# Performance work log

Hardware: AMD Instinct MI355X
Metric: run time of the kernel (lower is better)

## Reference

```python
import jax, jax.numpy as jnp
import numpy as np

B, N, D, V, Y = 4, 2048, 300, 50000, 20000
MAX_REL = 10
LN_EPS = 1e-5


def setup_inputs() -> dict:
    key = jax.random.key(0)
    k1, k2, k3, k4, k5 = jax.random.split(key, 5)
    M_s = jax.random.randint(k1, (B, N), 0, V, dtype=jnp.int64)
    s = 1.0 / np.sqrt(D)
    E_v = jax.random.normal(k2, (V, D), dtype=jnp.float32) * s
    E_v = E_v.at[0].set(0.0)  # padding_idx=0
    E_y = jax.random.normal(k3, (Y, D), dtype=jnp.float32) * s
    E_y = E_y.at[0].set(0.0)
    W_A = jax.random.normal(k4, (D, D), dtype=jnp.float32) * s
    W_O = jax.random.normal(k5, (D, D), dtype=jnp.float32) * s
    gamma = jnp.ones((D,), dtype=jnp.float32)
    beta = jnp.zeros((D,), dtype=jnp.float32)
    return {"M_s": M_s, "E_v": E_v, "E_y": E_y, "W_A": W_A, "W_O": W_O,
            "gamma": gamma, "beta": beta}


def reference(M_s, E_v, E_y, W_A, W_O, gamma, beta):
    # Embedding lookup (dropout is identity in eval / p=0)
    X = E_v[M_s]                                   # [B, N, D]
    Q = X                                          # self-attention mode (v_q=None)
    # weights = Q @ W_A @ X^T
    QW = jnp.einsum('bnd,de->bne', Q, W_A)         # [B, N, D]
    weights = jnp.einsum('bne,bme->bnm', QW, X)    # [B, N, N]
    # relative-distance bias (clipped |i-j|)
    r = jnp.arange(N)
    dist = jnp.clip(jnp.abs(r[None, :] - r[:, None]), 0, MAX_REL).astype(weights.dtype)
    weights = weights - dist
    # padding mask over context (key) positions
    mask = (M_s != 0)                              # [B, N]
    weights = jnp.where(mask[:, None, :], weights, -jnp.inf)
    A = jax.nn.softmax(weights, axis=-1)           # [B, N, N]
    # contextualized query + output projection
    Q_c = jnp.einsum('bnm,bmd->bnd', A, X) @ W_O   # [B, N, D]
    # residual + layernorm over D
    H = Q_c + Q
    mu = jnp.mean(H, axis=-1, keepdims=True)
    var = jnp.mean((H - mu) ** 2, axis=-1, keepdims=True)
    Hn = (H - mu) * jax.lax.rsqrt(var + LN_EPS) * gamma + beta
    # vocab projection over senses
    y_logits = Hn @ E_y.T                          # [B, N, Y]
    return y_logits, A
```

## Files before the change

kernel.cpp:

```cpp
#include <hip/hip_runtime.h>
#include <hip/hip_bf16.h>

#define B_ 4
#define N_ 2048
#define D_ 300
#define Y_ 20000
#define ROWS (B_*N_)

typedef __attribute__((ext_vector_type(8))) short bf16x8;
typedef __attribute__((ext_vector_type(4))) float f32x4;

__device__ __forceinline__ unsigned short f2bf(float f) {
  unsigned u = __float_as_uint(f);
  unsigned r = (u + 0x7FFFu + ((u >> 16) & 1u)) >> 16;
  return (unsigned short)r;
}

__device__ __forceinline__ void gl_lds16(const unsigned short* g, unsigned short* l) {
  __builtin_amdgcn_global_load_lds(
      (const __attribute__((address_space(1))) void*)g,
      (__attribute__((address_space(3))) void*)l, 16, 0, 0);
}

__global__ __launch_bounds__(256) void k_gather_pack(const int* __restrict__ M_s,
    const float* __restrict__ E_v, float* __restrict__ X,
    unsigned short* __restrict__ Xp) {
  __shared__ float xs[320];
  int row = blockIdx.x, tid = threadIdx.x;
  int tok = M_s[row];
  const float* src = E_v + (size_t)tok * D_;
  for (int d = tid; d < 320; d += 256) xs[d] = (d < D_) ? src[d] : 0.f;
  __syncthreads();
  float* dst = X + (size_t)row * D_;
  for (int d = tid; d < D_; d += 256) dst[d] = xs[d];
  if (tid < 40) {
    int kt = tid >> 2, j = tid & 3;
    int tile = row >> 7, fb = (row >> 4) & 7, rl = row & 15;
    unsigned short v[8];
    #pragma unroll
    for (int e = 0; e < 8; ++e) v[e] = f2bf(xs[kt*32 + j*8 + e]);
    size_t off_ = ((size_t)(tile*10 + kt))*4096 + fb*512 + rl*8 + j*128;
    ushort4* o = (ushort4*)&Xp[off_];
    o[0] = make_ushort4(v[0],v[1],v[2],v[3]);
    o[1] = make_ushort4(v[4],v[5],v[6],v[7]);
  }
}

__global__ __launch_bounds__(256) void k_pack(const float* __restrict__ src,
    unsigned short* __restrict__ dst, int nrows, int ncols, int KT) {
  int chunk = blockIdx.x;
  int tile = chunk / KT, kt = chunk - tile*KT;
  size_t obase = (size_t)chunk * 4096;
  #pragma unroll
  for (int p = 0; p < 2; ++p) {
    int idx = p*256 + threadIdx.x;
    int fb = idx >> 6, l = idx & 63;
    int row = tile*128 + fb*16 + (l & 15);
    int gk = kt*32 + (l >> 4)*8;
    unsigned short v[8];
    #pragma unroll
    for (int e = 0; e < 8; ++e) {
      int k = gk + e;
      float f = (row < nrows && k < ncols) ? src[(size_t)row*ncols + k] : 0.f;
      v[e] = f2bf(f);
    }
    ushort4* o = (ushort4*)&dst[obase + (size_t)idx*8];
    o[0] = make_ushort4(v[0],v[1],v[2],v[3]);
    o[1] = make_ushort4(v[4],v[5],v[6],v[7]);
  }
}

__global__ __launch_bounds__(256) void k_packT(const float* __restrict__ src,
    unsigned short* __restrict__ dst, int src_rows, int src_cols, int KT,
    size_t src_bstride, size_t dst_bchunks) {
  __shared__ float ls[32*133];
  int chunk = blockIdx.x, b = blockIdx.y, tid = threadIdx.x;
  const float* s = src + (size_t)b * src_bstride;
  unsigned short* d = dst + ((size_t)b * dst_bchunks + chunk) * 4096;
  int tile = chunk / KT, kt = chunk - tile*KT;
  int c0 = tile*128, k0 = kt*32;
  for (int i = tid; i < 4096; i += 256) {
    int r = i >> 7, c = i & 127;
    int sr = k0 + r, sc = c0 + c;
    ls[r*133 + c] = (sr < src_rows && sc < src_cols) ? s[(size_t)sr*src_cols + sc] : 0.f;
  }
  __syncthreads();
  #pragma unroll
  for (int p = 0; p < 2; ++p) {
    int idx = p*256 + tid;
    int fb = idx >> 6, l = idx & 63;
    int r = fb*16 + (l & 15);
    int kl = (l >> 4)*8;
    unsigned short v[8];
    #pragma unroll
    for (int e = 0; e < 8; ++e) v[e] = f2bf(ls[(kl + e)*133 + r]);
    ushort4* o = (ushort4*)&d[(size_t)idx*8];
    o[0] = make_ushort4(v[0],v[1],v[2],v[3]);
    o[1] = make_ushort4(v[4],v[5],v[6],v[7]);
  }
}

template<int EPI, bool NT, bool SWZ>
__global__ __launch_bounds__(512, 4) void k_gemm256(
    const unsigned short* __restrict__ Ap, const unsigned short* __restrict__ Bp,
    float* __restrict__ out, const int* __restrict__ Ms,
    int MTB, int NTB, int ncols)
{
  __shared__ __align__(16) union {
    unsigned short bstage[10][4096];
    float epi[64*132];
  } sm;
  int nt, mt, z;
  if (SWZ) {
    int wg = blockIdx.x;
    int cpx = (MTB*NTB) >> 3;
    int swz = (wg & 7)*cpx + (wg >> 3);
    mt = swz % MTB; nt = swz / MTB; z = 0;
  } else { nt = blockIdx.x; mt = blockIdx.y; z = blockIdx.z; }
  const int tid = threadIdx.x;
  const int wave = tid >> 6, lane = tid & 63;
  const int wm = wave >> 1, wn = wave & 1;
  const int mtile2 = (z*MTB + mt)*2 + (wm >> 1);
  const unsigned short* Ab = Ap + (size_t)mtile2 * 10 * 4096;
  const unsigned short* Bb = Bp + (size_t)(z*NTB + nt) * 10 * 4096;

  #pragma unroll
  for (int kt = 0; kt < 10; ++kt)
    gl_lds16(Bb + kt*4096 + wave*512 + lane*8, &sm.bstage[kt][wave*512]);

  const unsigned short* ga = Ab + ((wm & 1)*4)*512 + lane*8;
  __syncthreads();

  f32x4 acc[4][4] = {};
  #pragma unroll
  for (int kt = 0; kt < 10; ++kt) {
    bf16x8 a4[4], b4[4];
    #pragma unroll
    for (int i = 0; i < 4; ++i)
      a4[i] = *(const bf16x8*)(ga + kt*4096 + i*512);
    #pragma unroll
    for (int i = 0; i < 4; ++i)
      b4[i] = *(const bf16x8*)&sm.bstage[kt][(wn*4 + i)*512 + lane*8];
    #pragma unroll
    for (int mi = 0; mi < 4; ++mi)
      #pragma unroll
      for (int ni = 0; ni < 4; ++ni)
        acc[mi][ni] = __builtin_amdgcn_mfma_f32_16x16x32_bf16(
            a4[mi], b4[ni], acc[mi][ni], 0, 0, 0);
  }
  __syncthreads();

  const int lr0 = (lane >> 4) << 2;
  const int lc0 = wn*64 + (lane & 15);
  const size_t growbase = ((size_t)(z*MTB + mt)) << 8;
  #pragma unroll
  for (int h = 0; h < 4; ++h) {
    if (wm == h) {
      int tok[4];
      if (EPI == 1) {
        #pragma unroll
        for (int ni = 0; ni < 4; ++ni)
          tok[ni] = Ms[z*N_ + (nt<<7) + lc0 + ni*16];
      }
      #pragma unroll
      for (int mi = 0; mi < 4; ++mi) {
        #pragma unroll
        for (int ni = 0; ni < 4; ++ni) {
          int col = lc0 + ni*16;
          #pragma unroll
          for (int r = 0; r < 4; ++r) {
            int row = lr0 + mi*16 + r;
            float v = acc[mi][ni][r];
            if (EPI == 1) {
              int rb = (mt<<8) + h*64 + row;
              int gc = (nt<<7) + col;
              int dd = rb - gc; if (dd < 0) dd = -dd; if (dd > 10) dd = 10;
              v -= (float)dd;
              if (tok[ni] == 0) v = -3.0e38f;
            }
            sm.epi[row*132 + col] = v;
          }
        }
      }
    }
    __syncthreads();
    {
      const int r0 = tid >> 5;
      const int c4 = (tid & 31) << 2;
      const int gc = (nt << 7) + c4;
      #pragma unroll
      for (int rr = r0; rr < 64; rr += 16) {
        size_t grow = growbase + h*64 + rr;
        if (gc + 3 < ncols) {
          f32x4 v = *(const f32x4*)&sm.epi[rr*132 + c4];
          if (NT) __builtin_nontemporal_store(v, (f32x4*)&out[grow*(size_t)ncols + gc]);
          else    *(f32x4*)&out[grow*(size_t)ncols + gc] = v;
        } else {
          #pragma unroll
          for (int e = 0; e < 4; ++e) {
            int c = gc + e;
            if (c < ncols) {
              float v = sm.epi[rr*132 + c4 + e];
              if (NT) __builtin_nontemporal_store(v, &out[grow*(size_t)ncols + c]);
              else    out[grow*(size_t)ncols + c] = v;
            }
          }
        }
      }
    }
    __syncthreads();
  }
}

template<int EPI, bool NT, bool PACKOUT, bool SWZ>
__global__ __launch_bounds__(256) void k_gemm10(
    const unsigned short* __restrict__ Ap, const unsigned short* __restrict__ Bp,
    float* __restrict__ out, unsigned short* __restrict__ outp,
    const float* __restrict__ resid, const int* __restrict__ Ms,
    int KTd, int MTB, int NTB, int ncols)
{
  __shared__ __align__(16) union {
    unsigned short bstage[10][4096];
    float epi[64*132];
  } sm;
  int nt, mt, z;
  if (SWZ) {
    int nwg = MTB * NTB;
    int wg = blockIdx.x;
    int cpx = nwg >> 3;
    int swz = (wg & 7) * cpx + (wg >> 3);
    mt = swz % MTB; nt = swz / MTB; z = 0;
  } else {
    nt = blockIdx.x; mt = blockIdx.y; z = blockIdx.z;
  }
  const int tid = threadIdx.x;
  const int wave = tid >> 6, lane = tid & 63;
  const int wm = wave >> 1, wn = wave & 1;
  const unsigned short* Ab = Ap + (size_t)(z*MTB + mt) * 10 * 4096;
  const unsigned short* Bb = Bp + (size_t)(z*NTB + nt) * 10 * 4096;

  #pragma unroll
  for (int kt = 0; kt < 10; ++kt) {
    const unsigned short* gb = Bb + kt*4096 + wave*1024 + lane*8;
    unsigned short* lb = &sm.bstage[kt][wave*1024];
    gl_lds16(gb,       lb);
    gl_lds16(gb + 512, lb + 512);
  }

  const unsigned short* ga = Ab + (wm*4)*512 + lane*8;
  bf16x8 aA[4], aB[4];
  #pragma unroll
  for (int i = 0; i < 4; ++i) aA[i] = *(const bf16x8*)(ga + 0*4096 + i*512);
  #pragma unroll
  for (int i = 0; i < 4; ++i) aB[i] = *(const bf16x8*)(ga + 1*4096 + i*512);

  __syncthreads();

  f32x4 acc[4][4] = {};
  auto mfma_step = [&](int kt, const bf16x8* a) {
    bf16x8 bfr[4];
    #pragma unroll
    for (int i = 0; i < 4; ++i)
      bfr[i] = *(const bf16x8*)&sm.bstage[kt][(wn*4 + i)*512 + lane*8];
    #pragma unroll
    for (int mi = 0; mi < 4; ++mi)
      #pragma unroll
      for (int ni = 0; ni < 4; ++ni)
        acc[mi][ni] = __builtin_amdgcn_mfma_f32_16x16x32_bf16(
            a[mi], bfr[ni], acc[mi][ni], 0, 0, 0);
  };
  auto loadA = [&](int kt, bf16x8* d) {
    #pragma unroll
    for (int i = 0; i < 4; ++i) d[i] = *(const bf16x8*)(ga + kt*4096 + i*512);
  };

  #pragma unroll
  for (int kt = 0; kt < 10; kt += 2) {
    mfma_step(kt, aA);
    if (kt + 2 < 10) loadA(kt + 2, aA);
    mfma_step(kt + 1, aB);
    if (kt + 3 < 10) loadA(kt + 3, aB);
  }

  __syncthreads();

  const int lr0 = (lane >> 4) << 2;
  const int lc0 = wn*64 + (lane & 15);
  const size_t growbase = ((size_t)(z*MTB + mt)) << 7;
  #pragma unroll
  for (int h = 0; h < 2; ++h) {
    if (wm == h) {
      int tok[4];
      if (EPI == 1) {
        #pragma unroll
        for (int ni = 0; ni < 4; ++ni)
          tok[ni] = Ms[z*N_ + (nt<<7) + lc0 + ni*16];
      }
      #pragma unroll
      for (int mi = 0; mi < 4; ++mi) {
        #pragma unroll
        for (int ni = 0; ni < 4; ++ni) {
          int col = lc0 + ni*16;
          #pragma unroll
          for (int r = 0; r < 4; ++r) {
            int row = lr0 + mi*16 + r;
            float v = acc[mi][ni][r];
            if (EPI == 1) {
              int rb = (mt<<7) + h*64 + row;
              int gc = (nt<<7) + col;
              int dd = rb - gc; if (dd < 0) dd = -dd; if (dd > 10) dd = 10;
              v -= (float)dd;
              if (tok[ni] == 0) v = -3.0e38f;
            }
            sm.epi[row*132 + col] = v;
          }
        }
      }
    }
    __syncthreads();
    if (PACKOUT) {
      int prow = tid >> 2, pktq = tid & 3;
      int ktd = nt*4 + pktq;
      if (ktd < KTd) {
        int grl = h*64 + prow;
        int fb = grl >> 4, rl = grl & 15;
        size_t cbase = ((size_t)((z*MTB + mt)*KTd + ktd))*4096 + fb*512 + rl*8;
        #pragma unroll
        for (int oct = 0; oct < 4; ++oct) {
          unsigned short v[8];
          #pragma unroll
          for (int e = 0; e < 8; ++e)
            v[e] = f2bf(sm.epi[prow*132 + pktq*32 + oct*8 + e]);
          ushort4* o = (ushort4*)&outp[cbase + oct*128];
          o[0] = make_ushort4(v[0],v[1],v[2],v[3]);
          o[1] = make_ushort4(v[4],v[5],v[6],v[7]);
        }
      }
    } else {
      const int r0 = tid >> 5;
      const int c4 = (tid & 31) << 2;
      const int gc = (nt << 7) + c4;
      #pragma unroll
      for (int rr = r0; rr < 64; rr += 8) {
        size_t grow = growbase + h*64 + rr;
        if (gc + 3 < ncols) {
          f32x4 v = *(const f32x4*)&sm.epi[rr*132 + c4];
          if (EPI == 2) v += *(const f32x4*)&resid[grow*(size_t)ncols + gc];
          if (NT) __builtin_nontemporal_store(v, (f32x4*)&out[grow*(size_t)ncols + gc]);
          else    *(f32x4*)&out[grow*(size_t)ncols + gc] = v;
        } else {
          #pragma unroll
          for (int e = 0; e < 4; ++e) {
            int c = gc + e;
            if (c < ncols) {
              float v = sm.epi[rr*132 + c4 + e];
              if (EPI == 2) v += resid[grow*(size_t)ncols + c];
              if (NT) __builtin_nontemporal_store(v, &out[grow*(size_t)ncols + c]);
              else    out[grow*(size_t)ncols + c] = v;
            }
          }
        }
      }
    }
    __syncthreads();
  }
}

__global__ __launch_bounds__(256) void k_gemm64(
    const unsigned short* __restrict__ Ap, const unsigned short* __restrict__ Bp,
    unsigned short* __restrict__ outp, int KT, int KTd, int MTB, int NTB)
{
  __shared__ __align__(16) union {
    unsigned short stage[2][2][4096];
    float epi[64*132];
  } sm;
  const int nt = blockIdx.x, mt = blockIdx.y, z = blockIdx.z;
  const int tid = threadIdx.x;
  const int wave = tid >> 6, lane = tid & 63;
  const int wm = wave >> 1, wn = wave & 1;
  const unsigned short* Ab = Ap + (size_t)(z*MTB + mt) * KT * 4096;
  const unsigned short* Bb = Bp + (size_t)(z*NTB + nt) * KT * 4096;
  f32x4 acc[4][4] = {};

  auto stage = [&](int s, int kt) {
    const unsigned short* ga = Ab + kt*4096 + wave*1024 + lane*8;
    const unsigned short* gb = Bb + kt*4096 + wave*1024 + lane*8;
    unsigned short* la = &sm.stage[s][0][wave*1024];
    unsigned short* lb = &sm.stage[s][1][wave*1024];
    gl_lds16(ga,       la);
    gl_lds16(ga + 512, la + 512);
    gl_lds16(gb,       lb);
    gl_lds16(gb + 512, lb + 512);
  };

  stage(0, 0);
  __syncthreads();
  for (int kt = 0; kt < KT; ++kt) {
    int cur = kt & 1;
    if (kt + 1 < KT) stage(cur ^ 1, kt + 1);
    bf16x8 af[4], bfr[4];
    #pragma unroll
    for (int i = 0; i < 4; ++i)
      af[i] = *(const bf16x8*)&sm.stage[cur][0][(wm*4 + i)*512 + lane*8];
    #pragma unroll
    for (int i = 0; i < 4; ++i)
      bfr[i] = *(const bf16x8*)&sm.stage[cur][1][(wn*4 + i)*512 + lane*8];
    #pragma unroll
    for (int mi = 0; mi < 4; ++mi)
      #pragma unroll
      for (int ni = 0; ni < 4; ++ni)
        acc[mi][ni] = __builtin_amdgcn_mfma_f32_16x16x32_bf16(
            af[mi], bfr[ni], acc[mi][ni], 0, 0, 0);
    __syncthreads();
  }

  const int lr0 = (lane >> 4) << 2;
  const int lc0 = wn*64 + (lane & 15);
  #pragma unroll
  for (int h = 0; h < 2; ++h) {
    if (wm == h) {
      #pragma unroll
      for (int mi = 0; mi < 4; ++mi)
        #pragma unroll
        for (int ni = 0; ni < 4; ++ni) {
          int col = lc0 + ni*16;
          #pragma unroll
          for (int r = 0; r < 4; ++r)
            sm.epi[(lr0 + mi*16 + r)*132 + col] = acc[mi][ni][r];
        }
    }
    __syncthreads();
    {
      int prow = tid >> 2, pktq = tid & 3;
      int ktd = nt*4 + pktq;
      if (ktd < KTd) {
        int grl = h*64 + prow;
        int fb = grl >> 4, rl = grl & 15;
        size_t cbase = ((size_t)((z*MTB + mt)*KTd + ktd))*4096 + fb*512 + rl*8;
        #pragma unroll
        for (int oct = 0; oct < 4; ++oct) {
          unsigned short v[8];
          #pragma unroll
          for (int e = 0; e < 8; ++e)
            v[e] = f2bf(sm.epi[prow*132 + pktq*32 + oct*8 + e]);
          ushort4* o = (ushort4*)&outp[cbase + oct*128];
          o[0] = make_ushort4(v[0],v[1],v[2],v[3]);
          o[1] = make_ushort4(v[4],v[5],v[6],v[7]);
        }
      }
    }
    __syncthreads();
  }
}

__global__ __launch_bounds__(256) void k_softmax(float* __restrict__ S,
    unsigned short* __restrict__ Apk) {
  __shared__ float w[N_];
  __shared__ float red[4];
  int row = blockIdx.x, tid = threadIdx.x;
  float* sr = S + (size_t)row * N_;
  float vmax = -3.4e38f;
  for (int m = tid; m < N_; m += 256) { float v = sr[m]; w[m] = v; vmax = fmaxf(vmax, v); }
  #pragma unroll
  for (int off = 32; off; off >>= 1) vmax = fmaxf(vmax, __shfl_down(vmax, off, 64));
  if ((tid & 63) == 0) red[tid >> 6] = vmax;
  __syncthreads();
  vmax = fmaxf(fmaxf(red[0], red[1]), fmaxf(red[2], red[3]));
  float vsum = 0.f;
  for (int m = tid; m < N_; m += 256) {
    float e = __expf(w[m] - vmax);
    w[m] = e;
    vsum += e;
  }
  #pragma unroll
  for (int off = 32; off; off >>= 1) vsum += __shfl_down(vsum, off, 64);
  __syncthreads();
  if ((tid & 63) == 0) red[tid >> 6] = vsum;
  __syncthreads();
  float inv = 1.f / ((red[0] + red[1]) + (red[2] + red[3]));
  for (int m = tid; m < N_; m += 256)
    __builtin_nontemporal_store(w[m] * inv, &sr[m]);
  int kt = tid >> 2, j = tid & 3;
  int m0 = kt*32 + j*8;
  int fb = (row >> 4) & 7, rl = row & 15;
  unsigned short v[8];
  #pragma unroll
  for (int e = 0; e < 8; ++e) v[e] = f2bf(w[m0 + e] * inv);
  size_t off_ = ((size_t)((row >> 7)*64 + kt))*4096 + fb*512 + rl*8 + j*128;
  ushort4* o = (ushort4*)&Apk[off_];
  o[0] = make_ushort4(v[0],v[1],v[2],v[3]);
  o[1] = make_ushort4(v[4],v[5],v[6],v[7]);
}

__global__ __launch_bounds__(320) void k_ln_pack(const float* __restrict__ H,
    const float* __restrict__ gamma, const float* __restrict__ beta,
    unsigned short* __restrict__ Hp) {
  __shared__ float red[5];
  __shared__ float hs[320];
  int row = blockIdx.x, tid = threadIdx.x;
  float h = (tid < D_) ? H[(size_t)row*D_ + tid] : 0.f;
  float s = h;
  #pragma unroll
  for (int off = 32; off; off >>= 1) s += __shfl_down(s, off, 64);
  if ((tid & 63) == 0) red[tid >> 6] = s;
  __syncthreads();
  float mu = (red[0]+red[1]+red[2]+red[3]+red[4]) * (1.f/(float)D_);
  float dv = (tid < D_) ? (h - mu) : 0.f;
  float s2 = dv * dv;
  #pragma unroll
  for (int off = 32; off; off >>= 1) s2 += __shfl_down(s2, off, 64);
  __syncthreads();
  if ((tid & 63) == 0) red[tid >> 6] = s2;
  __syncthreads();
  float var = (red[0]+red[1]+red[2]+red[3]+red[4]) * (1.f/(float)D_);
  float rstd = rsqrtf(var + 1e-5f);
  hs[tid] = (tid < D_) ? (dv * rstd * gamma[tid] + beta[tid]) : 0.f;
  __syncthreads();
  if (tid < 40) {
    int kt = tid >> 2, j = tid & 3;
    int tile = row >> 7, fb = (row >> 4) & 7, rl = row & 15;
    unsigned short v[8];
    #pragma unroll
    for (int e = 0; e < 8; ++e) v[e] = f2bf(hs[kt*32 + j*8 + e]);
    size_t off_ = ((size_t)(tile*10 + kt))*4096 + fb*512 + rl*8 + j*128;
    ushort4* o = (ushort4*)&Hp[off_];
    o[0] = make_ushort4(v[0],v[1],v[2],v[3]);
    o[1] = make_ushort4(v[4],v[5],v[6],v[7]);
  }
}

extern "C" void kernel_launch(void* const* d_in, const int* in_sizes, int n_in,
                              void* d_out, int out_size, void* d_ws, size_t ws_size,
                              hipStream_t stream) {
  const int*   M_s   = (const int*)d_in[0];
  const float* E_v   = (const float*)d_in[1];
  const float* E_y   = (const float*)d_in[2];
  const float* W_A   = (const float*)d_in[3];
  const float* W_O   = (const float*)d_in[4];
  const float* gamma = (const float*)d_in[5];
  const float* beta  = (const float*)d_in[6];

  float* Yl = (float*)d_out;
  float* A  = Yl + (size_t)ROWS * Y_;

  float* X  = (float*)d_ws;
  float* QW = X  + (size_t)ROWS * D_;
  float* H  = QW + (size_t)ROWS * D_;
  unsigned short* Ep = (unsigned short*)(H + (size_t)ROWS * D_);
  unsigned short* Hpk = (unsigned short*)X;

  unsigned short* scr = (unsigned short*)(Yl + 100000000ull);
  unsigned short* Xp  = scr;
  unsigned short* QWp = Xp  + 2621440;
  unsigned short* Wap = QWp + 2621440;
  unsigned short* Wop = Wap + 122880;
  unsigned short* XTp = Wop + 122880;
  unsigned short* Cp  = XTp + 3145728;
  unsigned short* Apk = Cp  + 2621440;

  k_gather_pack<<<ROWS, 256, 0, stream>>>(M_s, E_v, X, Xp);
  k_packT <<<dim3(3*10,1), 256, 0, stream>>>(W_A, Wap, D_, D_, 10, 0, 0);
  k_gemm10<0,false,true,false><<<dim3(3,64,1), 256, 0, stream>>>(
      Xp, Wap, nullptr, QWp, nullptr, nullptr, 10, 64, 3, D_);
  k_gemm256<1,false,false><<<dim3(16,8,4), 512, 0, stream>>>(
      QWp, Xp, A, M_s, 8, 16, N_);
  k_softmax<<<ROWS, 256, 0, stream>>>(A, Apk);
  k_packT <<<dim3(3*64,4), 256, 0, stream>>>(X, XTp, N_, D_, 64, (size_t)N_*D_, 192);
  k_gemm64<<<dim3(3,16,4), 256, 0, stream>>>(Apk, XTp, Cp, 64, 10, 16, 3);
  k_packT <<<dim3(3*10,1), 256, 0, stream>>>(W_O, Wop, D_, D_, 10, 0, 0);
  k_gemm10<2,false,false,false><<<dim3(3,64,1), 256, 0, stream>>>(
      Cp, Wop, H, nullptr, X, nullptr, 0, 64, 3, D_);
  k_ln_pack<<<ROWS, 320, 0, stream>>>(H, gamma, beta, Hpk);
  k_pack  <<<157*10, 256, 0, stream>>>(E_y, Ep, Y_, D_, 10);
  k_gemm256<0,true,true><<<dim3(157*32,1,1), 512, 0, stream>>>(
      Hpk, Ep, Yl, nullptr, 32, 157, Y_);
}
```

Measured before the change: 376.0 us.

## Store GEMM epilogue directly from registers and vectorize softmax row handling

The 256-row GEMM epilogue no longer stages the accumulator tile through shared memory with four barrier-separated passes. Each lane now writes its scalar results straight to global memory, which removes the LDS round trip and the barriers but replaces wide coalesced stores with strided scalar stores. The softmax kernel holds each row in registers as two float4 vectors, computes exp once, and uses separate reduction buffers. This drops one barrier and the repeated LDS reads and writes.

```diff
diff --git a/kernel.cpp b/kernel.cpp
--- a/kernel.cpp
+++ b/kernel.cpp
@@ -106,10 +106,7 @@
     float* __restrict__ out, const int* __restrict__ Ms,
     int MTB, int NTB, int ncols)
 {
-  __shared__ __align__(16) union {
-    unsigned short bstage[10][4096];
-    float epi[64*132];
-  } sm;
+  __shared__ __align__(16) unsigned short bstage[10][4096];
   int nt, mt, z;
   if (SWZ) {
     int wg = blockIdx.x;
@@ -126,7 +123,7 @@
 
   #pragma unroll
   for (int kt = 0; kt < 10; ++kt)
-    gl_lds16(Bb + kt*4096 + wave*512 + lane*8, &sm.bstage[kt][wave*512]);
+    gl_lds16(Bb + kt*4096 + wave*512 + lane*8, &bstage[kt][wave*512]);
 
   const unsigned short* ga = Ab + ((wm & 1)*4)*512 + lane*8;
   __syncthreads();
@@ -140,7 +137,7 @@
       a4[i] = *(const bf16x8*)(ga + kt*4096 + i*512);
     #pragma unroll
     for (int i = 0; i < 4; ++i)
-      b4[i] = *(const bf16x8*)&sm.bstage[kt][(wn*4 + i)*512 + lane*8];
+      b4[i] = *(const bf16x8*)&bstage[kt][(wn*4 + i)*512 + lane*8];
     #pragma unroll
     for (int mi = 0; mi < 4; ++mi)
       #pragma unroll
@@ -148,67 +145,37 @@
         acc[mi][ni] = __builtin_amdgcn_mfma_f32_16x16x32_bf16(
             a4[mi], b4[ni], acc[mi][ni], 0, 0, 0);
   }
-  __syncthreads();
 
   const int lr0 = (lane >> 4) << 2;
   const int lc0 = wn*64 + (lane & 15);
-  const size_t growbase = ((size_t)(z*MTB + mt)) << 8;
-  #pragma unroll
-  for (int h = 0; h < 4; ++h) {
-    if (wm == h) {
-      int tok[4];
-      if (EPI == 1) {
-        #pragma unroll
-        for (int ni = 0; ni < 4; ++ni)
-          tok[ni] = Ms[z*N_ + (nt<<7) + lc0 + ni*16];
-      }
-      #pragma unroll
-      for (int mi = 0; mi < 4; ++mi) {
-        #pragma unroll
-        for (int ni = 0; ni < 4; ++ni) {
-          int col = lc0 + ni*16;
-          #pragma unroll
-          for (int r = 0; r < 4; ++r) {
-            int row = lr0 + mi*16 + r;
-            float v = acc[mi][ni][r];
-            if (EPI == 1) {
-              int rb = (mt<<8) + h*64 + row;
-              int gc = (nt<<7) + col;
-              int dd = rb - gc; if (dd < 0) dd = -dd; if (dd > 10) dd = 10;
-              v -= (float)dd;
-              if (tok[ni] == 0) v = -3.0e38f;
-            }
-            sm.epi[row*132 + col] = v;
-          }
+  const size_t grow0 = ((size_t)(z*MTB + mt))*256 + wm*64 + lr0;
+  const int rb0 = mt*256 + wm*64 + lr0;
+  int tok[4];
+  if (EPI == 1) {
+    #pragma unroll
+    for (int ni = 0; ni < 4; ++ni)
+      tok[ni] = Ms[z*N_ + (nt<<7) + lc0 + ni*16];
+  }
+  #pragma unroll
+  for (int ni = 0; ni < 4; ++ni) {
+    int gc = (nt << 7) + lc0 + ni*16;
+    if (gc >= ncols) continue;
+    #pragma unroll
+    for (int mi = 0; mi < 4; ++mi) {
+      #pragma unroll
+      for (int r = 0; r < 4; ++r) {
+        float v = acc[mi][ni][r];
+        if (EPI == 1) {
+          int rb = rb0 + mi*16 + r;
+          int dd = rb - gc; if (dd < 0) dd = -dd; if (dd > 10) dd = 10;
+          v -= (float)dd;
+          if (tok[ni] == 0) v = -3.0e38f;
         }
+        size_t go = (grow0 + mi*16 + r) * (size_t)ncols + gc;
+        if (NT) __builtin_nontemporal_store(v, &out[go]);
+        else    out[go] = v;
       }
     }
-    __syncthreads();
-    {
-      const int r0 = tid >> 5;
-      const int c4 = (tid & 31) << 2;
-      const int gc = (nt << 7) + c4;
-      #pragma unroll
-      for (int rr = r0; rr < 64; rr += 16) {
-        size_t grow = growbase + h*64 + rr;
-        if (gc + 3 < ncols) {
-          f32x4 v = *(const f32x4*)&sm.epi[rr*132 + c4];
-          if (NT) __builtin_nontemporal_store(v, (f32x4*)&out[grow*(size_t)ncols + gc]);
-          else    *(f32x4*)&out[grow*(size_t)ncols + gc] = v;
-        } else {
-          #pragma unroll
-          for (int e = 0; e < 4; ++e) {
-            int c = gc + e;
-            if (c < ncols) {
-              float v = sm.epi[rr*132 + c4 + e];
-              if (NT) __builtin_nontemporal_store(v, &out[grow*(size_t)ncols + c]);
-              else    out[grow*(size_t)ncols + c] = v;
-            }
-          }
-        }
-      }
-    }
-    __syncthreads();
   }
 }
 
@@ -456,30 +423,34 @@
 __global__ __launch_bounds__(256) void k_softmax(float* __restrict__ S,
     unsigned short* __restrict__ Apk) {
   __shared__ float w[N_];
-  __shared__ float red[4];
+  __shared__ float redm[4], reds[4];
   int row = blockIdx.x, tid = threadIdx.x;
   float* sr = S + (size_t)row * N_;
-  float vmax = -3.4e38f;
-  for (int m = tid; m < N_; m += 256) { float v = sr[m]; w[m] = v; vmax = fmaxf(vmax, v); }
+  f32x4 v0 = ((const f32x4*)sr)[tid];
+  f32x4 v1 = ((const f32x4*)sr)[tid + 256];
+  float vmax = fmaxf(fmaxf(fmaxf(v0.x, v0.y), fmaxf(v0.z, v0.w)),
+                     fmaxf(fmaxf(v1.x, v1.y), fmaxf(v1.z, v1.w)));
   #pragma unroll
   for (int off = 32; off; off >>= 1) vmax = fmaxf(vmax, __shfl_down(vmax, off, 64));
-  if ((tid & 63) == 0) red[tid >> 6] = vmax;
-  __syncthreads();
-  vmax = fmaxf(fmaxf(red[0], red[1]), fmaxf(red[2], red[3]));
-  float vsum = 0.f;
-  for (int m = tid; m < N_; m += 256) {
-    float e = __expf(w[m] - vmax);
-    w[m] = e;
-    vsum += e;
-  }
+  if ((tid & 63) == 0) redm[tid >> 6] = vmax;
+  __syncthreads();
+  vmax = fmaxf(fmaxf(redm[0], redm[1]), fmaxf(redm[2], redm[3]));
+  f32x4 e0, e1;
+  e0.x = __expf(v0.x - vmax); e0.y = __expf(v0.y - vmax);
+  e0.z = __expf(v0.z - vmax); e0.w = __expf(v0.w - vmax);
+  e1.x = __expf(v1.x - vmax); e1.y = __expf(v1.y - vmax);
+  e1.z = __expf(v1.z - vmax); e1.w = __expf(v1.w - vmax);
+  ((f32x4*)w)[tid] = e0;
+  ((f32x4*)w)[tid + 256] = e1;
+  float vsum = (e0.x + e0.y + e0.z + e0.w) + (e1.x + e1.y + e1.z + e1.w);
   #pragma unroll
   for (int off = 32; off; off >>= 1) vsum += __shfl_down(vsum, off, 64);
-  __syncthreads();
-  if ((tid & 63) == 0) red[tid >> 6] = vsum;
-  __syncthreads();
-  float inv = 1.f / ((red[0] + red[1]) + (red[2] + red[3]));
-  for (int m = tid; m < N_; m += 256)
-    __builtin_nontemporal_store(w[m] * inv, &sr[m]);
+  if ((tid & 63) == 0) reds[tid >> 6] = vsum;
+  __syncthreads();
+  float inv = 1.f / ((reds[0] + reds[1]) + (reds[2] + reds[3]));
+  f32x4 o0 = e0 * inv, o1 = e1 * inv;
+  __builtin_nontemporal_store(o0, &((f32x4*)sr)[tid]);
+  __builtin_nontemporal_store(o1, &((f32x4*)sr)[tid + 256]);
   int kt = tid >> 2, j = tid & 3;
   int m0 = kt*32 + j*8;
   int fb = (row >> 4) & 7, rl = row & 15;
```

New measurement: 426.5 us. +13.4%, slower.
